# Kernel tuning notes

Hardware: AMD Instinct MI355X
Metric: run time of the kernel (lower is better)

The kernel has to match this reference:

```python
import jax, jax.numpy as jnp
import numpy as np

B, S, C, L, H = 128, 8, 120, 469, 64


def setup_inputs() -> dict:
    key = jax.random.key(0)
    kx, kk, kq, kv = jax.random.split(key, 4)
    scale = 1.0 / np.sqrt(L)
    x = jax.random.normal(kx, (B, S, C, L), dtype=jnp.float32)
    # nn.Linear(L, H, bias=False): y = x @ W^T with W:[H,L]; store as [L,H] so y = x @ W
    Wk = jax.random.normal(kk, (L, H), dtype=jnp.float32) * scale
    Wq = jax.random.normal(kq, (L, H), dtype=jnp.float32) * scale
    Wv = jax.random.normal(kv, (L, H), dtype=jnp.float32) * scale
    return {"x": x, "Wk": Wk, "Wq": Wq, "Wv": Wv}


def reference(x, Wk, Wq, Wv):
    b, s, c, l = x.shape
    h = Wk.shape[-1]
    # torch: x.view(S_, B, C_, L_) -- a raw reshape, not a permute
    xs = x.reshape(s, b, c, l)
    k = xs @ Wk  # (s, b, c, h)
    q = xs @ Wq
    v = xs @ Wv
    wei = jnp.einsum('sbch,sbdh->sbcd', q, k) * (h ** -0.5)
    wei = jax.nn.softmax(wei, axis=-1)  # dropout = identity in eval
    out = jnp.einsum('sbcd,sbdh->sbch', wei, v)  # (s, b, c, h)
    # torch: matrices.view(B, S_, C_, head_size) -- raw reshape again
    return out.reshape(b, s, c, h)
```

## Files before the change

kernel.cpp:

```cpp
#include <hip/hip_runtime.h>
#include <hip/hip_bf16.h>

typedef __attribute__((ext_vector_type(8))) short bf16x8;
typedef __attribute__((ext_vector_type(4))) float f32x4;
typedef __attribute__((ext_vector_type(4))) short short4v;
typedef unsigned short ushort_t;

#define CC 120
#define LL 469
#define HH 64

constexpr int NBATCH = 1024;
constexpr int KSTEPS = (LL + 31) / 32;

constexpr int XB_STRIDE   = 40;
constexpr int XBUF_SHORTS = CC * XB_STRIDE;
constexpr int WBUF_SHORTS = 192 * 40;
constexpr int WBUF_BYTES  = WBUF_SHORTS * 2;
constexpr int SMEM_BYTES  = 2 * XBUF_SHORTS * 2 + 2 * WBUF_BYTES;
constexpr int WIMG_BYTES  = KSTEPS * WBUF_BYTES;

__device__ __forceinline__ ushort_t f2bf(float f) {
  __hip_bfloat16 h = __float2bfloat16(f);
  return __builtin_bit_cast(ushort_t, h);
}

__device__ __forceinline__ void gload_lds16(const void* g, void* l) {
  __builtin_amdgcn_global_load_lds(
      (const __attribute__((address_space(1))) unsigned int*)g,
      (__attribute__((address_space(3))) unsigned int*)l, 16, 0, 0);
}

__device__ __forceinline__ char* sptr(char* base, int row, int stride, int byteoff) {
  return base + row * stride + (byteoff ^ ((row & 7) << 4));
}

__global__ void prep_w(const float* __restrict__ Wk, const float* __restrict__ Wq,
                       const float* __restrict__ Wv, ushort_t* __restrict__ wimg) {
  int idx = blockIdx.x * 256 + threadIdx.x;
  int t = idx / (192 * 40);
  int rem = idx % (192 * 40);
  int col = rem / 40;
  int kk = rem % 40;
  int k = t * 32 + kk;
  int wsel = col >> 6, h = col & 63;
  const float* wp = (wsel == 0) ? Wk : (wsel == 1) ? Wq : Wv;
  float v = (kk < 32 && k < LL) ? wp[(size_t)k * HH + h] : 0.f;
  wimg[idx] = f2bf(v);
}

template <bool WIMG>
__global__ __launch_bounds__(256, 3)
void fused_regional_head(const float* __restrict__ x,
                         const float* __restrict__ Wk,
                         const float* __restrict__ Wq,
                         const float* __restrict__ Wv,
                         const ushort_t* __restrict__ wimg,
                         float* __restrict__ out) {
  __shared__ char smem[SMEM_BYTES];
  const int tid = threadIdx.x;
  const int lane = tid & 63;
  const int wv = tid >> 6;
  const int lr = lane & 15;
  const int lg = lane >> 4;
  const int batch = blockIdx.x;
  const size_t xbase = (size_t)batch * CC * LL;

  ushort_t* Xb = (ushort_t*)smem;
  ushort_t* Wl = (ushort_t*)(smem + 2 * XBUF_SHORTS * 2);

  const int skk = tid & 31;
  const int sr0 = tid >> 5;

  auto xload = [&](int t, float* v) {
    const int k = t * 32 + skk;
    const bool kok = k < LL;
#pragma unroll
    for (int i = 0; i < 15; ++i) {
      v[i] = 0.f;
      if (kok) v[i] = x[xbase + (size_t)(i * 8 + sr0) * LL + k];
    }
  };
  auto xwrite = [&](int buf, const float* v) {
    ushort_t* xb = Xb + buf * XBUF_SHORTS;
#pragma unroll
    for (int i = 0; i < 15; ++i)
      xb[(i * 8 + sr0) * XB_STRIDE + skk] = f2bf(v[i]);
  };

  auto stage_w = [&](int buf, int t) {
    ushort_t* wb = Wl + buf * WBUF_SHORTS;
    if constexpr (WIMG) {
      const char* src = (const char*)(wimg + t * WBUF_SHORTS);
#pragma unroll
      for (int i = 0; i < 4; ++i) {
        int c = wv + 4 * i;
        if (c < 15) gload_lds16(src + c * 1024 + lane * 16, (char*)wb + c * 1024);
      }
    } else {
      const int k0 = t * 32;
#pragma unroll
      for (int j = 0; j < 24; ++j) {
        int idx = j * 256 + tid;
        int col = idx >> 5, kk = idx & 31;
        int k = k0 + kk;
        int wsel = col >> 6, h = col & 63;
        const float* wp = (wsel == 0) ? Wk : (wsel == 1) ? Wq : Wv;
        float v = (k < LL) ? wp[(size_t)k * HH + h] : 0.f;
        wb[col * 40 + kk] = f2bf(v);
      }
    }
  };

  f32x4 acc[2][12];
#pragma unroll
  for (int m = 0; m < 2; ++m)
#pragma unroll
    for (int n = 0; n < 12; ++n) acc[m][n] = (f32x4){0.f, 0.f, 0.f, 0.f};

  {
    float v0[15];
    xload(0, v0);
    xwrite(0, v0);
  }
  stage_w(0, 0);

  const int row0 = wv * 32 + lr;
  const int row1 = wv * 32 + 16 + lr;
  const bool r1ok = row1 < CC;

  float vx[15];
  for (int t = 0; t < KSTEPS; ++t) {
    __syncthreads();
    if (t + 1 < KSTEPS) {
      xload(t + 1, vx);
      stage_w((t + 1) & 1, t + 1);
    }
    const ushort_t* xb = Xb + (t & 1) * XBUF_SHORTS;
    const ushort_t* wb = Wl + (t & 1) * WBUF_SHORTS;
    bf16x8 a0 = *(const bf16x8*)(xb + row0 * XB_STRIDE + lg * 8);
    bf16x8 a1;
    if (r1ok) a1 = *(const bf16x8*)(xb + row1 * XB_STRIDE + lg * 8);
    else { bf16x8 z = {0,0,0,0,0,0,0,0}; a1 = z; }
#pragma unroll
    for (int n = 0; n < 12; ++n) {
      bf16x8 b = *(const bf16x8*)(wb + (n * 16 + lr) * 40 + lg * 8);
      acc[0][n] = __builtin_amdgcn_mfma_f32_16x16x32_bf16(a0, b, acc[0][n], 0, 0, 0);
      acc[1][n] = __builtin_amdgcn_mfma_f32_16x16x32_bf16(a1, b, acc[1][n], 0, 0, 0);
    }
    if (t + 1 < KSTEPS) xwrite((t + 1) & 1, vx);
  }
  __syncthreads();

  char* Qb = smem;
  char* Kb = smem + 16384;
  char* Vb = smem + 32768;
  char* Pb = smem;
#pragma unroll
  for (int mt = 0; mt < 2; ++mt) {
#pragma unroll
    for (int r = 0; r < 4; ++r) {
      int row = wv * 32 + mt * 16 + lg * 4 + r;
#pragma unroll
      for (int n = 0; n < 4; ++n) {
        *(ushort_t*)sptr(Kb, row, 128, (n * 16 + lr) * 2) = f2bf(acc[mt][n][r]);
        *(ushort_t*)sptr(Qb, row, 128, (n * 16 + lr) * 2) = f2bf(acc[mt][4 + n][r]);
      }
    }
#pragma unroll
    for (int n = 0; n < 4; ++n) {
      short4v pk;
#pragma unroll
      for (int r = 0; r < 4; ++r) pk[r] = (short)f2bf(acc[mt][8 + n][r]);
      *(short4v*)sptr(Vb, n * 16 + lr, 256, (wv * 32 + mt * 16 + lg * 4) * 2) = pk;
    }
  }
  __syncthreads();

  f32x4 accw[2][8];
#pragma unroll
  for (int m = 0; m < 2; ++m)
#pragma unroll
    for (int n = 0; n < 8; ++n) accw[m][n] = (f32x4){0.f, 0.f, 0.f, 0.f};
#pragma unroll
  for (int ks = 0; ks < 2; ++ks) {
    bf16x8 a0 = *(const bf16x8*)sptr(Qb, wv * 32 + lr, 128, ks * 64 + lg * 16);
    bf16x8 a1 = *(const bf16x8*)sptr(Qb, wv * 32 + 16 + lr, 128, ks * 64 + lg * 16);
#pragma unroll
    for (int n = 0; n < 8; ++n) {
      bf16x8 b = *(const bf16x8*)sptr(Kb, n * 16 + lr, 128, ks * 64 + lg * 16);
      accw[0][n] = __builtin_amdgcn_mfma_f32_16x16x32_bf16(a0, b, accw[0][n], 0, 0, 0);
      accw[1][n] = __builtin_amdgcn_mfma_f32_16x16x32_bf16(a1, b, accw[1][n], 0, 0, 0);
    }
  }
  __syncthreads();

#pragma unroll
  for (int mt = 0; mt < 2; ++mt)
#pragma unroll
    for (int r = 0; r < 4; ++r) {
      float l[8];
      float m = -1e30f;
#pragma unroll
      for (int n = 0; n < 8; ++n) {
        float v = accw[mt][n][r] * 0.125f;
        if (n == 7 && lr >= 8) v = -1e30f;
        l[n] = v;
        m = fmaxf(m, v);
      }
#pragma unroll
      for (int off = 1; off < 16; off <<= 1) m = fmaxf(m, __shfl_xor(m, off));
      float s = 0.f;
#pragma unroll
      for (int n = 0; n < 8; ++n) {
        float p = __expf(l[n] - m);
        l[n] = p;
        s += p;
      }
#pragma unroll
      for (int off = 1; off < 16; off <<= 1) s += __shfl_xor(s, off);
      float inv = 1.f / s;
      int row = wv * 32 + mt * 16 + lg * 4 + r;
#pragma unroll
      for (int n = 0; n < 8; ++n)
        *(ushort_t*)sptr(Pb, row, 256, (n * 16 + lr) * 2) = f2bf(l[n] * inv);
    }

  f32x4 acco[2][4];
#pragma unroll
  for (int m = 0; m < 2; ++m)
#pragma unroll
    for (int n = 0; n < 4; ++n) acco[m][n] = (f32x4){0.f, 0.f, 0.f, 0.f};
#pragma unroll
  for (int ks = 0; ks < 4; ++ks) {
    bf16x8 a0 = *(const bf16x8*)sptr(Pb, wv * 32 + lr, 256, ks * 64 + lg * 16);
    bf16x8 a1 = *(const bf16x8*)sptr(Pb, wv * 32 + 16 + lr, 256, ks * 64 + lg * 16);
#pragma unroll
    for (int n = 0; n < 4; ++n) {
      bf16x8 b = *(const bf16x8*)sptr(Vb, n * 16 + lr, 256, ks * 64 + lg * 16);
      acco[0][n] = __builtin_amdgcn_mfma_f32_16x16x32_bf16(a0, b, acco[0][n], 0, 0, 0);
      acco[1][n] = __builtin_amdgcn_mfma_f32_16x16x32_bf16(a1, b, acco[1][n], 0, 0, 0);
    }
  }

  __syncthreads();
  float* Ob = (float*)smem;
#pragma unroll
  for (int mt = 0; mt < 2; ++mt)
#pragma unroll
    for (int r = 0; r < 4; ++r) {
      int row = wv * 32 + mt * 16 + lg * 4 + r;
      if (row < CC) {
#pragma unroll
        for (int n = 0; n < 4; ++n)
          Ob[row * 68 + n * 16 + lr] = acco[mt][n][r];
      }
    }
  __syncthreads();
  const size_t obase = (size_t)batch * CC * HH;
#pragma unroll
  for (int i = 0; i < 8; ++i) {
    int idx = i * 256 + tid;
    if (idx < 1920) {
      int row = idx >> 4;
      int c4 = (idx & 15) * 4;
      f32x4 v = *(const f32x4*)(Ob + row * 68 + c4);
      *(f32x4*)(out + obase + (size_t)idx * 4) = v;
    }
  }
}

extern "C" void kernel_launch(void* const* d_in, const int* in_sizes, int n_in,
                              void* d_out, int out_size, void* d_ws, size_t ws_size,
                              hipStream_t stream) {
  (void)in_sizes; (void)n_in; (void)out_size;
  const float* x  = (const float*)d_in[0];
  const float* Wk = (const float*)d_in[1];
  const float* Wq = (const float*)d_in[2];
  const float* Wv = (const float*)d_in[3];
  float* out = (float*)d_out;
  if (ws_size >= (size_t)WIMG_BYTES && d_ws != nullptr) {
    ushort_t* wimg = (ushort_t*)d_ws;
    prep_w<<<450, 256, 0, stream>>>(Wk, Wq, Wv, wimg);
    fused_regional_head<true><<<NBATCH, 256, 0, stream>>>(x, Wk, Wq, Wv, wimg, out);
  } else {
    fused_regional_head<false><<<NBATCH, 256, 0, stream>>>(x, Wk, Wq, Wv, nullptr, out);
  }
}
```

Measured before the change: 81.32 us.

## Load X directly into MFMA A-fragments from global, bypassing LDS staging

```diff
diff --git a/kernel.cpp b/kernel.cpp
--- a/kernel.cpp
+++ b/kernel.cpp
@@ -3,6 +3,7 @@
 
 typedef __attribute__((ext_vector_type(8))) short bf16x8;
 typedef __attribute__((ext_vector_type(4))) float f32x4;
+typedef float f32x4u __attribute__((ext_vector_type(4), aligned(4)));
 typedef __attribute__((ext_vector_type(4))) short short4v;
 typedef unsigned short ushort_t;
 
@@ -13,11 +14,9 @@
 constexpr int NBATCH = 1024;
 constexpr int KSTEPS = (LL + 31) / 32;
 
-constexpr int XB_STRIDE   = 40;
-constexpr int XBUF_SHORTS = CC * XB_STRIDE;
 constexpr int WBUF_SHORTS = 192 * 40;
 constexpr int WBUF_BYTES  = WBUF_SHORTS * 2;
-constexpr int SMEM_BYTES  = 2 * XBUF_SHORTS * 2 + 2 * WBUF_BYTES;
+constexpr int SMEM_BYTES  = 49152;
 constexpr int WIMG_BYTES  = KSTEPS * WBUF_BYTES;
 
 __device__ __forceinline__ ushort_t f2bf(float f) {
@@ -66,26 +65,34 @@
   const int batch = blockIdx.x;
   const size_t xbase = (size_t)batch * CC * LL;
 
-  ushort_t* Xb = (ushort_t*)smem;
-  ushort_t* Wl = (ushort_t*)(smem + 2 * XBUF_SHORTS * 2);
-
-  const int skk = tid & 31;
-  const int sr0 = tid >> 5;
-
-  auto xload = [&](int t, float* v) {
-    const int k = t * 32 + skk;
-    const bool kok = k < LL;
-#pragma unroll
-    for (int i = 0; i < 15; ++i) {
-      v[i] = 0.f;
-      if (kok) v[i] = x[xbase + (size_t)(i * 8 + sr0) * LL + k];
-    }
-  };
-  auto xwrite = [&](int buf, const float* v) {
-    ushort_t* xb = Xb + buf * XBUF_SHORTS;
-#pragma unroll
-    for (int i = 0; i < 15; ++i)
-      xb[(i * 8 + sr0) * XB_STRIDE + skk] = f2bf(v[i]);
+  ushort_t* Wl = (ushort_t*)smem;
+
+  const int row0 = wv * 32 + lr;
+  const int row1 = wv * 32 + 16 + lr;
+  const bool r1ok = row1 < CC;
+  const float* xr0 = x + xbase + (size_t)row0 * LL;
+  const float* xr1 = x + xbase + (size_t)row1 * LL;
+
+  auto loadX = [&](int t, f32x4u* c) {
+    const f32x4u z = (f32x4u){0.f, 0.f, 0.f, 0.f};
+    if (t == KSTEPS - 1) {
+#pragma unroll
+      for (int j = 0; j < 4; ++j) {
+        int ka = 448 + lg * 8 + j, kb = ka + 4;
+        c[0][j] = (ka < LL) ? xr0[ka] : 0.f;
+        c[1][j] = (kb < LL) ? xr0[kb] : 0.f;
+        c[2][j] = (r1ok && ka < LL) ? xr1[ka] : 0.f;
+        c[3][j] = (r1ok && kb < LL) ? xr1[kb] : 0.f;
+      }
+    } else {
+      const int off = t * 32 + lg * 8;
+      c[0] = *(const f32x4u*)(xr0 + off);
+      c[1] = *(const f32x4u*)(xr0 + off + 4);
+      if (r1ok) {
+        c[2] = *(const f32x4u*)(xr1 + off);
+        c[3] = *(const f32x4u*)(xr1 + off + 4);
+      } else { c[2] = z; c[3] = z; }
+    }
   };
 
   auto stage_w = [&](int buf, int t) {
@@ -118,39 +125,34 @@
 #pragma unroll
     for (int n = 0; n < 12; ++n) acc[m][n] = (f32x4){0.f, 0.f, 0.f, 0.f};
 
-  {
-    float v0[15];
-    xload(0, v0);
-    xwrite(0, v0);
-  }
+  f32x4u cx[4], nx[4];
+  loadX(0, cx);
   stage_w(0, 0);
-
-  const int row0 = wv * 32 + lr;
-  const int row1 = wv * 32 + 16 + lr;
-  const bool r1ok = row1 < CC;
-
-  float vx[15];
+  __syncthreads();
+
+#pragma unroll
   for (int t = 0; t < KSTEPS; ++t) {
-    __syncthreads();
     if (t + 1 < KSTEPS) {
-      xload(t + 1, vx);
+      loadX(t + 1, nx);
       stage_w((t + 1) & 1, t + 1);
     }
-    const ushort_t* xb = Xb + (t & 1) * XBUF_SHORTS;
+    bf16x8 a0, a1;
+#pragma unroll
+    for (int j = 0; j < 4; ++j) {
+      a0[j] = (short)f2bf(cx[0][j]); a0[4 + j] = (short)f2bf(cx[1][j]);
+      a1[j] = (short)f2bf(cx[2][j]); a1[4 + j] = (short)f2bf(cx[3][j]);
+    }
     const ushort_t* wb = Wl + (t & 1) * WBUF_SHORTS;
-    bf16x8 a0 = *(const bf16x8*)(xb + row0 * XB_STRIDE + lg * 8);
-    bf16x8 a1;
-    if (r1ok) a1 = *(const bf16x8*)(xb + row1 * XB_STRIDE + lg * 8);
-    else { bf16x8 z = {0,0,0,0,0,0,0,0}; a1 = z; }
 #pragma unroll
     for (int n = 0; n < 12; ++n) {
       bf16x8 b = *(const bf16x8*)(wb + (n * 16 + lr) * 40 + lg * 8);
       acc[0][n] = __builtin_amdgcn_mfma_f32_16x16x32_bf16(a0, b, acc[0][n], 0, 0, 0);
       acc[1][n] = __builtin_amdgcn_mfma_f32_16x16x32_bf16(a1, b, acc[1][n], 0, 0, 0);
     }
-    if (t + 1 < KSTEPS) xwrite((t + 1) & 1, vx);
-  }
-  __syncthreads();
+    __syncthreads();
+#pragma unroll
+    for (int j = 0; j < 4; ++j) cx[j] = nx[j];
+  }
 
   char* Qb = smem;
   char* Kb = smem + 16384;
```

Result: slower. 152.2 us (+87.2%).

## Deepen projection pipeline with two-step x prefetch and manual waitcnt barriers

Applied to the files above, without the earlier changes.

```diff
diff --git a/kernel.cpp b/kernel.cpp
--- a/kernel.cpp
+++ b/kernel.cpp
@@ -15,10 +15,11 @@
 
 constexpr int XB_STRIDE   = 40;
 constexpr int XBUF_SHORTS = CC * XB_STRIDE;
-constexpr int WBUF_SHORTS = 192 * 40;
-constexpr int WBUF_BYTES  = WBUF_SHORTS * 2;
-constexpr int SMEM_BYTES  = 2 * XBUF_SHORTS * 2 + 2 * WBUF_BYTES;
-constexpr int WIMG_BYTES  = KSTEPS * WBUF_BYTES;
+constexpr int WB_SHORTS   = 8192;
+constexpr int X_BYTES     = 2 * XBUF_SHORTS * 2;
+constexpr int SMEM_BYTES  = X_BYTES + 2 * WB_SHORTS * 2;
+constexpr int WIMG_SHORTS = KSTEPS * WB_SHORTS;
+constexpr int WIMG_BYTES  = WIMG_SHORTS * 2;
 
 __device__ __forceinline__ ushort_t f2bf(float f) {
   __hip_bfloat16 h = __float2bfloat16(f);
@@ -38,14 +39,16 @@
 __global__ void prep_w(const float* __restrict__ Wk, const float* __restrict__ Wq,
                        const float* __restrict__ Wv, ushort_t* __restrict__ wimg) {
   int idx = blockIdx.x * 256 + threadIdx.x;
-  int t = idx / (192 * 40);
-  int rem = idx % (192 * 40);
-  int col = rem / 40;
-  int kk = rem % 40;
-  int k = t * 32 + kk;
-  int wsel = col >> 6, h = col & 63;
-  const float* wp = (wsel == 0) ? Wk : (wsel == 1) ? Wq : Wv;
-  float v = (kk < 32 && k < LL) ? wp[(size_t)k * HH + h] : 0.f;
+  int t = idx / WB_SHORTS;
+  int r = idx % WB_SHORTS;
+  int col = r / 40, kk = r % 40;
+  float v = 0.f;
+  if (r < 192 * 40 && kk < 32) {
+    int k = t * 32 + kk;
+    int wsel = col >> 6, h = col & 63;
+    const float* wp = (wsel == 0) ? Wk : (wsel == 1) ? Wq : Wv;
+    if (k < LL) v = wp[(size_t)k * HH + h];
+  }
   wimg[idx] = f2bf(v);
 }
 
@@ -66,49 +69,47 @@
   const int batch = blockIdx.x;
   const size_t xbase = (size_t)batch * CC * LL;
 
-  ushort_t* Xb = (ushort_t*)smem;
-  ushort_t* Wl = (ushort_t*)(smem + 2 * XBUF_SHORTS * 2);
+  ushort_t* Xl = (ushort_t*)smem;
+  ushort_t* Wl = (ushort_t*)(smem + X_BYTES);
 
   const int skk = tid & 31;
   const int sr0 = tid >> 5;
 
   auto xload = [&](int t, float* v) {
-    const int k = t * 32 + skk;
-    const bool kok = k < LL;
-#pragma unroll
-    for (int i = 0; i < 15; ++i) {
-      v[i] = 0.f;
-      if (kok) v[i] = x[xbase + (size_t)(i * 8 + sr0) * LL + k];
-    }
-  };
-  auto xwrite = [&](int buf, const float* v) {
-    ushort_t* xb = Xb + buf * XBUF_SHORTS;
+    int k = t * 32 + skk;
+    int kc = (k < LL) ? k : (LL - 1);
 #pragma unroll
     for (int i = 0; i < 15; ++i)
-      xb[(i * 8 + sr0) * XB_STRIDE + skk] = f2bf(v[i]);
-  };
-
-  auto stage_w = [&](int buf, int t) {
-    ushort_t* wb = Wl + buf * WBUF_SHORTS;
-    if constexpr (WIMG) {
-      const char* src = (const char*)(wimg + t * WBUF_SHORTS);
-#pragma unroll
-      for (int i = 0; i < 4; ++i) {
-        int c = wv + 4 * i;
-        if (c < 15) gload_lds16(src + c * 1024 + lane * 16, (char*)wb + c * 1024);
-      }
-    } else {
-      const int k0 = t * 32;
-#pragma unroll
-      for (int j = 0; j < 24; ++j) {
-        int idx = j * 256 + tid;
-        int col = idx >> 5, kk = idx & 31;
-        int k = k0 + kk;
-        int wsel = col >> 6, h = col & 63;
-        const float* wp = (wsel == 0) ? Wk : (wsel == 1) ? Wq : Wv;
-        float v = (k < LL) ? wp[(size_t)k * HH + h] : 0.f;
-        wb[col * 40 + kk] = f2bf(v);
-      }
+      v[i] = x[xbase + (size_t)(i * 8 + sr0) * LL + kc];
+  };
+  auto xwrite = [&](int buf, const float* v, int t) {
+    const bool ok = (t * 32 + skk) < LL;
+    ushort_t* xb = Xl + buf * XBUF_SHORTS;
+#pragma unroll
+    for (int i = 0; i < 15; ++i)
+      xb[(i * 8 + sr0) * XB_STRIDE + skk] = f2bf(ok ? v[i] : 0.f);
+  };
+  auto stage_w_fast = [&](int buf, int t) {
+    const char* src = (const char*)(wimg + (size_t)t * WB_SHORTS);
+    char* dst = (char*)(Wl + buf * WB_SHORTS);
+#pragma unroll
+    for (int i = 0; i < 4; ++i) {
+      int c = wv + 4 * i;
+      gload_lds16(src + c * 1024 + lane * 16, dst + c * 1024);
+    }
+  };
+  auto stage_w_slow = [&](int buf, int t) {
+    ushort_t* wb = Wl + buf * WB_SHORTS;
+    const int k0 = t * 32;
+#pragma unroll
+    for (int j = 0; j < 24; ++j) {
+      int idx = j * 256 + tid;
+      int col = idx >> 5, kk = idx & 31;
+      int k = k0 + kk;
+      int wsel = col >> 6, h = col & 63;
+      const float* wp = (wsel == 0) ? Wk : (wsel == 1) ? Wq : Wv;
+      float v = (k < LL) ? wp[(size_t)k * HH + h] : 0.f;
+      wb[col * 40 + kk] = f2bf(v);
     }
   };
 
@@ -117,27 +118,14 @@
   for (int m = 0; m < 2; ++m)
 #pragma unroll
     for (int n = 0; n < 12; ++n) acc[m][n] = (f32x4){0.f, 0.f, 0.f, 0.f};
-
-  {
-    float v0[15];
-    xload(0, v0);
-    xwrite(0, v0);
-  }
-  stage_w(0, 0);
 
   const int row0 = wv * 32 + lr;
   const int row1 = wv * 32 + 16 + lr;
   const bool r1ok = row1 < CC;
 
-  float vx[15];
-  for (int t = 0; t < KSTEPS; ++t) {
-    __syncthreads();
-    if (t + 1 < KSTEPS) {
-      xload(t + 1, vx);
-      stage_w((t + 1) & 1, t + 1);
-    }
-    const ushort_t* xb = Xb + (t & 1) * XBUF_SHORTS;
-    const ushort_t* wb = Wl + (t & 1) * WBUF_SHORTS;
+  auto compute = [&](int t) {
+    const ushort_t* xb = Xl + (t & 1) * XBUF_SHORTS;
+    const ushort_t* wb = Wl + (t & 1) * WB_SHORTS;
     bf16x8 a0 = *(const bf16x8*)(xb + row0 * XB_STRIDE + lg * 8);
     bf16x8 a1;
     if (r1ok) a1 = *(const bf16x8*)(xb + row1 * XB_STRIDE + lg * 8);
@@ -148,7 +136,53 @@
       acc[0][n] = __builtin_amdgcn_mfma_f32_16x16x32_bf16(a0, b, acc[0][n], 0, 0, 0);
       acc[1][n] = __builtin_amdgcn_mfma_f32_16x16x32_bf16(a1, b, acc[1][n], 0, 0, 0);
     }
-    if (t + 1 < KSTEPS) xwrite((t + 1) & 1, vx);
+  };
+
+  if constexpr (WIMG) {
+    float xA[15], xB[15];
+    stage_w_fast(0, 0);
+    __builtin_amdgcn_sched_barrier(0);
+    xload(0, xA);
+    xload(1, xB);
+    xwrite(0, xA, 0);
+    asm volatile("s_waitcnt vmcnt(15) lgkmcnt(0)" ::: "memory");
+    __builtin_amdgcn_s_barrier();
+    __builtin_amdgcn_sched_barrier(0);
+
+#pragma unroll
+    for (int t = 0; t < KSTEPS; ++t) {
+      float* fill = (t & 1) ? xB : xA;
+      float* cons = (t & 1) ? xA : xB;
+      if (t + 1 < KSTEPS) {
+        stage_w_fast((t + 1) & 1, t + 1);
+        __builtin_amdgcn_sched_barrier(0);
+      }
+      if (t + 2 < KSTEPS) xload(t + 2, fill);
+      compute(t);
+      if (t + 1 < KSTEPS) xwrite((t + 1) & 1, cons, t + 1);
+      if (t + 1 < KSTEPS) {
+        if (t == KSTEPS - 2) {
+          asm volatile("s_waitcnt vmcnt(0) lgkmcnt(0)" ::: "memory");
+        } else {
+          asm volatile("s_waitcnt vmcnt(15) lgkmcnt(0)" ::: "memory");
+        }
+        __builtin_amdgcn_s_barrier();
+        __builtin_amdgcn_sched_barrier(0);
+      }
+    }
+  } else {
+    float vx[15];
+    xload(0, vx);
+    xwrite(0, vx, 0);
+    stage_w_slow(0, 0);
+    __syncthreads();
+#pragma unroll
+    for (int t = 0; t < KSTEPS; ++t) {
+      if (t + 1 < KSTEPS) xload(t + 1, vx);
+      compute(t);
+      if (t + 1 < KSTEPS) { xwrite((t + 1) & 1, vx, t + 1); stage_w_slow((t + 1) & 1, t + 1); }
+      __syncthreads();
+    }
   }
   __syncthreads();
 
@@ -281,7 +315,7 @@
   float* out = (float*)d_out;
   if (ws_size >= (size_t)WIMG_BYTES && d_ws != nullptr) {
     ushort_t* wimg = (ushort_t*)d_ws;
-    prep_w<<<450, 256, 0, stream>>>(Wk, Wq, Wv, wimg);
+    prep_w<<<480, 256, 0, stream>>>(Wk, Wq, Wv, wimg);
     fused_regional_head<true><<<NBATCH, 256, 0, stream>>>(x, Wk, Wq, Wv, wimg, out);
   } else {
     fused_regional_head<false><<<NBATCH, 256, 0, stream>>>(x, Wk, Wq, Wv, nullptr, out);
```

Result: slower. 216.3 us (+166.0%).
